# Optimization experiments

Hardware: AMD Instinct MI355X
Metric: run time of the kernel (lower is better)

## Reference

```python
import jax, jax.numpy as jnp
import numpy as np

B = 4096      # batch of users
D = 128       # embedding_dim
NA = 128      # num_anchors
AD = 128      # anchor_dim
NU = 100000   # num_users
NI = 50000    # num_items


def setup_inputs() -> dict:
    key = jax.random.key(0)
    ks = jax.random.split(key, 10)
    s = 0.05
    return {
        "user_indices": jax.random.randint(ks[0], (B,), 0, NU),
        "pos_item_indices": jax.random.randint(ks[1], (B,), 0, NI),
        "user_table": jax.random.normal(ks[2], (NU, D), dtype=jnp.float32) * s,
        "item_table": jax.random.normal(ks[3], (NI, D), dtype=jnp.float32) * s,
        "ln1_g": jnp.ones((D,), jnp.float32),
        "ln1_b": jnp.zeros((D,), jnp.float32),
        "send_W": jax.random.normal(ks[4], (D, AD), dtype=jnp.float32) * s,
        "send_a": jax.random.normal(ks[5], (2 * AD,), dtype=jnp.float32) * s,
        "anchors": jax.random.normal(ks[6], (NA, AD), dtype=jnp.float32) * s,
        "ln2_g": jnp.ones((NA,), jnp.float32),
        "ln2_b": jnp.zeros((NA,), jnp.float32),
        "recv_W": jax.random.normal(ks[7], (NA, D), dtype=jnp.float32) * s,
        "recv_a": jax.random.normal(ks[8], (2 * D,), dtype=jnp.float32) * s,
    }


def _layernorm(x, g, b, eps=1e-5):
    m = jnp.mean(x, axis=-1, keepdims=True)
    v = jnp.mean((x - m) ** 2, axis=-1, keepdims=True)
    return (x - m) * jax.lax.rsqrt(v + eps) * g + b


def _fca(x, W, a):
    # FullyConnectedAttention: score[i,j] = [t_i ; t_j] . a = t_i.a1 + t_j.a2
    # (decomposed form of the torch repeat/cat -> same math, no [B,B,2F] tensor)
    t = x @ W                       # [B, F]
    f = t.shape[-1]
    a1, a2 = a[:f], a[f:]
    e = (t @ a1)[:, None] + (t @ a2)[None, :]   # [B, B]
    w = jax.nn.softmax(e, axis=1)
    return w @ t                    # [B, F]


def reference(user_indices, pos_item_indices, user_table, item_table,
              ln1_g, ln1_b, send_W, send_a, anchors, ln2_g, ln2_b,
              recv_W, recv_a):
    u = user_table[user_indices]                 # [B, D]
    # AdaptiveAnchorConvolution
    nf = _layernorm(u, ln1_g, ln1_b)             # feature_norm
    sent = _fca(nf, send_W, send_a)              # send_attention -> [B, AD]
    ap = sent @ anchors.T                        # anchor projection [B, NA]
    na = _layernorm(ap, ln2_g, ln2_b)            # anchor_norm
    rec = _fca(na, recv_W, recv_a)               # receive_attention -> [B, D]
    ue = u + jnp.sin(rec)                        # residual + sin
    pos = item_table[pos_item_indices]           # [B, D]
    preds = ue @ item_table.T                    # [B, NI]
    return preds, ue, pos
```

## Files before the change

### kernel.cpp

```cpp
#include <hip/hip_runtime.h>
#include <hip/hip_bf16.h>

#define BB   4096
#define DD   128
#define NII  50000

typedef __attribute__((ext_vector_type(8))) short  bf8_t;
typedef __attribute__((ext_vector_type(4))) float  f4_t;
typedef __attribute__((ext_vector_type(4))) unsigned short us4_t;
typedef __attribute__((ext_vector_type(4))) float  fl4_t;

static __device__ __forceinline__ unsigned short f2bf(float f) {
    unsigned u = __float_as_uint(f);
    u += 0x7fffu + ((u >> 16) & 1u);
    return (unsigned short)(u >> 16);
}

static __device__ __forceinline__ void gload_lds16(const void* g, void* lds) {
    __builtin_amdgcn_global_load_lds(
        (const __attribute__((address_space(1))) void*)g,
        (__attribute__((address_space(3))) void*)lds, 16, 0, 0);
}

__global__ __launch_bounds__(128) void k1_embed_send(
    const int* __restrict__ uidx, const float* __restrict__ utab,
    const float* __restrict__ g1, const float* __restrict__ b1,
    const float* __restrict__ sendW, const float* __restrict__ senda,
    float* __restrict__ t_out, float* __restrict__ s2_out)
{
    __shared__ float sb[128];
    __shared__ float nf[128];
    const int row = blockIdx.x;
    const int tid = threadIdx.x;
    const long urow = uidx[row];
    const float x = utab[urow * 128 + tid];

    sb[tid] = x; __syncthreads();
    for (int s = 64; s > 0; s >>= 1) { if (tid < s) sb[tid] += sb[tid + s]; __syncthreads(); }
    const float mean = sb[0] * (1.0f / 128.0f); __syncthreads();
    const float dv = x - mean;
    sb[tid] = dv * dv; __syncthreads();
    for (int s = 64; s > 0; s >>= 1) { if (tid < s) sb[tid] += sb[tid + s]; __syncthreads(); }
    const float var = sb[0] * (1.0f / 128.0f);
    const float rs = rsqrtf(var + 1e-5f);
    nf[tid] = dv * rs * g1[tid] + b1[tid];
    __syncthreads();

    float acc = 0.f;
    #pragma unroll 8
    for (int d = 0; d < 128; ++d) acc += nf[d] * sendW[d * 128 + tid];
    t_out[row * 128 + tid] = acc;

    const float p = acc * senda[128 + tid];
    __syncthreads();
    sb[tid] = p; __syncthreads();
    for (int s = 64; s > 0; s >>= 1) { if (tid < s) sb[tid] += sb[tid + s]; __syncthreads(); }
    if (tid == 0) s2_out[row] = sb[0];
}

__global__ __launch_bounds__(256) void k2b_colsum(
    const float* __restrict__ t, const float* __restrict__ s2,
    float* __restrict__ partial)
{
    __shared__ float ew[128];
    __shared__ float sb[256];
    const int tid = threadIdx.x;

    float m = -1e30f;
    for (int i = tid; i < BB; i += 256) m = fmaxf(m, s2[i]);
    sb[tid] = m; __syncthreads();
    for (int s = 128; s > 0; s >>= 1) { if (tid < s) sb[tid] = fmaxf(sb[tid], sb[tid + s]); __syncthreads(); }
    m = sb[0]; __syncthreads();

    const int rbase = blockIdx.x * 128;
    if (tid < 128) ew[tid] = __expf(s2[rbase + tid] - m);
    __syncthreads();
    const int col = tid & 127, half = tid >> 7;
    float acc = 0.f;
    for (int j = half; j < 128; j += 2)
        acc += ew[j] * t[(rbase + j) * 128 + col];
    sb[tid] = acc; __syncthreads();
    if (tid < 128) partial[blockIdx.x * 128 + tid] = sb[tid] + sb[tid + 128];
}

__global__ __launch_bounds__(128) void k2c_finish(
    const float* __restrict__ partial, const float* __restrict__ s2,
    const float* __restrict__ anchors, const float* __restrict__ g2,
    const float* __restrict__ b2, const float* __restrict__ recvW,
    float* __restrict__ r_out)
{
    __shared__ float sent[128];
    __shared__ float na_s[128];
    __shared__ float sb[128];
    const int tid = threadIdx.x;

    float m = -1e30f;
    for (int i = tid; i < BB; i += 128) m = fmaxf(m, s2[i]);
    sb[tid] = m; __syncthreads();
    for (int s = 64; s > 0; s >>= 1) { if (tid < s) sb[tid] = fmaxf(sb[tid], sb[tid + s]); __syncthreads(); }
    m = sb[0]; __syncthreads();
    float sum = 0.f;
    for (int i = tid; i < BB; i += 128) sum += __expf(s2[i] - m);
    sb[tid] = sum; __syncthreads();
    for (int s = 64; s > 0; s >>= 1) { if (tid < s) sb[tid] += sb[tid + s]; __syncthreads(); }
    const float S = sb[0]; __syncthreads();

    float acc = 0.f;
    for (int b = 0; b < 32; ++b) acc += partial[b * 128 + tid];
    sent[tid] = acc / S;
    __syncthreads();
    float ap = 0.f;
    for (int c = 0; c < 128; ++c) ap += sent[c] * anchors[tid * 128 + c];
    sb[tid] = ap; __syncthreads();
    for (int s = 64; s > 0; s >>= 1) { if (tid < s) sb[tid] += sb[tid + s]; __syncthreads(); }
    const float mean = sb[0] * (1.0f / 128.0f); __syncthreads();
    const float dv = ap - mean;
    sb[tid] = dv * dv; __syncthreads();
    for (int s = 64; s > 0; s >>= 1) { if (tid < s) sb[tid] += sb[tid + s]; __syncthreads(); }
    const float var = sb[0] * (1.0f / 128.0f);
    const float rs = rsqrtf(var + 1e-5f);
    na_s[tid] = dv * rs * g2[tid] + b2[tid];
    __syncthreads();
    float t2 = 0.f;
    for (int k = 0; k < 128; ++k) t2 += na_s[k] * recvW[k * 128 + tid];
    r_out[tid] = sinf(t2);
}

__global__ __launch_bounds__(256) void k3_ue_pos(
    const int* __restrict__ uidx, const float* __restrict__ utab,
    const int* __restrict__ pidx, const float* __restrict__ itab,
    const float* __restrict__ r, float* __restrict__ ue_out,
    float* __restrict__ pos_out, unsigned short* __restrict__ uebf)
{
    const int gid = blockIdx.x * 256 + threadIdx.x;
    const int i = gid >> 7, d = gid & 127;
    const float rv = r[d];
    const float u = utab[(long)uidx[i] * 128 + d];
    const float ue = u + rv;
    ue_out[gid] = ue;
    uebf[gid] = f2bf(ue);
    pos_out[gid] = itab[(long)pidx[i] * 128 + d];
}

__global__ __launch_bounds__(256) void k3b_cvt_item(
    const float* __restrict__ itab, unsigned short* __restrict__ ibf)
{
    const int gid = blockIdx.x * 256 + threadIdx.x;
    const fl4_t v = *(const fl4_t*)(itab + (long)gid * 4);
    us4_t o;
    o.x = f2bf(v.x); o.y = f2bf(v.y); o.z = f2bf(v.z); o.w = f2bf(v.w);
    *(us4_t*)(ibf + (long)gid * 4) = o;
}

__global__ __launch_bounds__(512, 2) void k4_gemm(
    const unsigned short* __restrict__ uebf,
    const unsigned short* __restrict__ ibf,
    float* __restrict__ preds)
{
    __shared__ unsigned short lA[256 * 128];
    __shared__ unsigned short lB[256 * 128];

    const int tid = threadIdx.x;
    const int wave = tid >> 6, lane = tid & 63;
    const int l15 = lane & 15, kg = lane >> 4;
    const int col0 = blockIdx.x * 256;
    const int row0 = blockIdx.y * 256;

    #pragma unroll
    for (int i = 0; i < 8; ++i) {
        const int o  = (i * 512 + tid) * 16;
        const int r  = o >> 8;
        const int ch = (o >> 4) & 15;
        const int sw = ch ^ (r & 15);
        gload_lds16(uebf + (size_t)(row0 + r) * 128 + sw * 8,
                    (char*)lA + i * 8192 + wave * 1024);
        const int bc = (col0 + r) < NII ? (col0 + r) : (NII - 1);
        gload_lds16(ibf + (size_t)bc * 128 + sw * 8,
                    (char*)lB + i * 8192 + wave * 1024);
    }

    const int wr = wave >> 2, wcn = wave & 3;

    f4_t acc[8][4];
    #pragma unroll
    for (int m = 0; m < 8; ++m)
        #pragma unroll
        for (int n = 0; n < 4; ++n) acc[m][n] = (f4_t){0.f, 0.f, 0.f, 0.f};

    __syncthreads();

    #pragma unroll
    for (int kk = 0; kk < 4; ++kk) {
        const int c = kk * 4 + kg;
        bf8_t a[8], b[4];
        #pragma unroll
        for (int m = 0; m < 8; ++m) {
            const int r = wr * 128 + m * 16 + l15;
            a[m] = *(const bf8_t*)((const char*)lA + r * 256 + (c ^ (r & 15)) * 16);
        }
        #pragma unroll
        for (int n = 0; n < 4; ++n) {
            const int r = wcn * 64 + n * 16 + l15;
            b[n] = *(const bf8_t*)((const char*)lB + r * 256 + (c ^ (r & 15)) * 16);
        }
        #pragma unroll
        for (int m = 0; m < 8; ++m)
            #pragma unroll
            for (int n = 0; n < 4; ++n)
                acc[m][n] = __builtin_amdgcn_mfma_f32_16x16x32_bf16(b[n], a[m], acc[m][n], 0, 0, 0);
    }

    #pragma unroll
    for (int m = 0; m < 8; ++m) {
        const long grow = row0 + wr * 128 + m * 16 + l15;
        #pragma unroll
        for (int n = 0; n < 4; ++n) {
            const int gcol = col0 + wcn * 64 + n * 16 + kg * 4;
            if (gcol < NII)
                *(fl4_t*)(preds + grow * NII + gcol) = acc[m][n];
        }
    }
}

extern "C" void kernel_launch(void* const* d_in, const int* in_sizes, int n_in,
                              void* d_out, int out_size, void* d_ws, size_t ws_size,
                              hipStream_t stream) {
    const int*   uidx   = (const int*)  d_in[0];
    const int*   pidx   = (const int*)  d_in[1];
    const float* utab   = (const float*)d_in[2];
    const float* itab   = (const float*)d_in[3];
    const float* g1     = (const float*)d_in[4];
    const float* b1     = (const float*)d_in[5];
    const float* sendW  = (const float*)d_in[6];
    const float* senda  = (const float*)d_in[7];
    const float* anchors= (const float*)d_in[8];
    const float* g2     = (const float*)d_in[9];
    const float* b2     = (const float*)d_in[10];
    const float* recvW  = (const float*)d_in[11];

    char* ws = (char*)d_ws;
    float* t_ws    = (float*)(ws + 0);
    float* s2_ws   = (float*)(ws + 2097152);
    float* part_ws = (float*)(ws + 2113600);
    float* r_ws    = (float*)(ws + 2129984);
    unsigned short* uebf = (unsigned short*)(ws + 2130496);
    unsigned short* ibf  = (unsigned short*)(ws + 3179072);

    float* preds   = (float*)d_out;
    float* ue_out  = preds + (long)BB * NII;
    float* pos_out = ue_out + BB * DD;

    k3b_cvt_item<<<6250, 256, 0, stream>>>(itab, ibf);
    k1_embed_send<<<4096, 128, 0, stream>>>(uidx, utab, g1, b1, sendW, senda, t_ws, s2_ws);
    k2b_colsum<<<32, 256, 0, stream>>>(t_ws, s2_ws, part_ws);
    k2c_finish<<<1, 128, 0, stream>>>(part_ws, s2_ws, anchors, g2, b2, recvW, r_ws);
    k3_ue_pos<<<2048, 256, 0, stream>>>(uidx, utab, pidx, itab, r_ws, ue_out, pos_out, uebf);
    k4_gemm<<<dim3(196, 16, 1), 512, 0, stream>>>(uebf, ibf, preds);
}
```

Baseline: 243.4 us.

## Make GEMM blocks loop over item column tiles with double-buffered B prefetch

The preds GEMM now gives each block 4–5 consecutive 128-column item tiles instead of one 256-column tile. The block's 256-row user tile stays resident in LDS for the whole loop. The next item tile is prefetched into a second LDS buffer while the current tile's MFMAs and output stores run, synchronised with a partial vmcnt wait. The goal is to cut redundant A-tile loads, overlap B loads with compute and stores, and shrink the grid from 3136 to 1536 blocks to reduce tail imbalance. In exchange, each block does more serial work and relies on the hand-tuned vmcnt count being correct.

```diff
diff --git a/kernel.cpp b/kernel.cpp
--- a/kernel.cpp
+++ b/kernel.cpp
@@ -4,6 +4,7 @@
 #define BB   4096
 #define DD   128
 #define NII  50000
+#define NT128 391
 
 typedef __attribute__((ext_vector_type(8))) short  bf8_t;
 typedef __attribute__((ext_vector_type(4))) float  f4_t;
@@ -158,67 +159,93 @@
     float* __restrict__ preds)
 {
     __shared__ unsigned short lA[256 * 128];
-    __shared__ unsigned short lB[256 * 128];
+    __shared__ unsigned short lB[2][128 * 128];
 
     const int tid = threadIdx.x;
     const int wave = tid >> 6, lane = tid & 63;
     const int l15 = lane & 15, kg = lane >> 4;
-    const int col0 = blockIdx.x * 256;
+    const int bx = blockIdx.x;
     const int row0 = blockIdx.y * 256;
+    const int nt0 = bx * 4 + (bx < 7 ? bx : 7);
+    const int ns  = 4 + (bx < 7 ? 1 : 0);
 
     #pragma unroll
     for (int i = 0; i < 8; ++i) {
-        const int o  = (i * 512 + tid) * 16;
-        const int r  = o >> 8;
-        const int ch = (o >> 4) & 15;
-        const int sw = ch ^ (r & 15);
+        const int o = (i * 512 + tid) * 16, r = o >> 8, ch = (o >> 4) & 15, sw = ch ^ (r & 15);
         gload_lds16(uebf + (size_t)(row0 + r) * 128 + sw * 8,
                     (char*)lA + i * 8192 + wave * 1024);
-        const int bc = (col0 + r) < NII ? (col0 + r) : (NII - 1);
-        gload_lds16(ibf + (size_t)bc * 128 + sw * 8,
-                    (char*)lB + i * 8192 + wave * 1024);
     }
+    {
+        const int c0 = nt0 * 128;
+        #pragma unroll
+        for (int i = 0; i < 4; ++i) {
+            const int o = (i * 512 + tid) * 16, r = o >> 8, ch = (o >> 4) & 15, sw = ch ^ (r & 15);
+            const int bc = (c0 + r) < NII ? (c0 + r) : (NII - 1);
+            gload_lds16(ibf + (size_t)bc * 128 + sw * 8,
+                        (char*)lB[0] + i * 8192 + wave * 1024);
+        }
+    }
+    asm volatile("s_waitcnt vmcnt(0)" ::: "memory");
+    __builtin_amdgcn_sched_barrier(0);
+    __builtin_amdgcn_s_barrier();
 
     const int wr = wave >> 2, wcn = wave & 3;
 
-    f4_t acc[8][4];
-    #pragma unroll
-    for (int m = 0; m < 8; ++m)
-        #pragma unroll
-        for (int n = 0; n < 4; ++n) acc[m][n] = (f4_t){0.f, 0.f, 0.f, 0.f};
-
-    __syncthreads();
-
-    #pragma unroll
-    for (int kk = 0; kk < 4; ++kk) {
-        const int c = kk * 4 + kg;
-        bf8_t a[8], b[4];
+    for (int j = 0; j < ns; ++j) {
+        if (j + 1 < ns) {
+            const int c0n = (nt0 + j + 1) * 128;
+            char* dst = (char*)lB[(j + 1) & 1];
+            #pragma unroll
+            for (int i = 0; i < 4; ++i) {
+                const int o = (i * 512 + tid) * 16, r = o >> 8, ch = (o >> 4) & 15, sw = ch ^ (r & 15);
+                const int bc = (c0n + r) < NII ? (c0n + r) : (NII - 1);
+                gload_lds16(ibf + (size_t)bc * 128 + sw * 8, dst + i * 8192 + wave * 1024);
+            }
+        }
+        const unsigned short* bb = lB[j & 1];
+
+        f4_t acc[8][2];
+        #pragma unroll
+        for (int m = 0; m < 8; ++m)
+            #pragma unroll
+            for (int n = 0; n < 2; ++n) acc[m][n] = (f4_t){0.f, 0.f, 0.f, 0.f};
+
+        #pragma unroll
+        for (int kk = 0; kk < 4; ++kk) {
+            const int c = kk * 4 + kg;
+            bf8_t a[8], b[2];
+            #pragma unroll
+            for (int m = 0; m < 8; ++m) {
+                const int r = wr * 128 + m * 16 + l15;
+                a[m] = *(const bf8_t*)((const char*)lA + r * 256 + (c ^ (r & 15)) * 16);
+            }
+            #pragma unroll
+            for (int n = 0; n < 2; ++n) {
+                const int r = wcn * 32 + n * 16 + l15;
+                b[n] = *(const bf8_t*)((const char*)bb + r * 256 + (c ^ (r & 15)) * 16);
+            }
+            #pragma unroll
+            for (int m = 0; m < 8; ++m)
+                #pragma unroll
+                for (int n = 0; n < 2; ++n)
+                    acc[m][n] = __builtin_amdgcn_mfma_f32_16x16x32_bf16(b[n], a[m], acc[m][n], 0, 0, 0);
+        }
+
+        const int col0 = (nt0 + j) * 128;
         #pragma unroll
         for (int m = 0; m < 8; ++m) {
-            const int r = wr * 128 + m * 16 + l15;
-            a[m] = *(const bf8_t*)((const char*)lA + r * 256 + (c ^ (r & 15)) * 16);
-        }
-        #pragma unroll
-        for (int n = 0; n < 4; ++n) {
-            const int r = wcn * 64 + n * 16 + l15;
-            b[n] = *(const bf8_t*)((const char*)lB + r * 256 + (c ^ (r & 15)) * 16);
-        }
-        #pragma unroll
-        for (int m = 0; m < 8; ++m)
-            #pragma unroll
-            for (int n = 0; n < 4; ++n)
-                acc[m][n] = __builtin_amdgcn_mfma_f32_16x16x32_bf16(b[n], a[m], acc[m][n], 0, 0, 0);
-    }
-
-    #pragma unroll
-    for (int m = 0; m < 8; ++m) {
-        const long grow = row0 + wr * 128 + m * 16 + l15;
-        #pragma unroll
-        for (int n = 0; n < 4; ++n) {
-            const int gcol = col0 + wcn * 64 + n * 16 + kg * 4;
-            if (gcol < NII)
-                *(fl4_t*)(preds + grow * NII + gcol) = acc[m][n];
-        }
+            const long grow = row0 + wr * 128 + m * 16 + l15;
+            #pragma unroll
+            for (int n = 0; n < 2; ++n) {
+                const int gcol = col0 + wcn * 32 + n * 16 + kg * 4;
+                if (gcol < NII)
+                    *(fl4_t*)(preds + grow * NII + gcol) = acc[m][n];
+            }
+        }
+
+        asm volatile("s_waitcnt vmcnt(16)" ::: "memory");
+        __builtin_amdgcn_sched_barrier(0);
+        __builtin_amdgcn_s_barrier();
     }
 }
 
@@ -255,5 +282,5 @@
     k2b_colsum<<<32, 256, 0, stream>>>(t_ws, s2_ws, part_ws);
     k2c_finish<<<1, 128, 0, stream>>>(part_ws, s2_ws, anchors, g2, b2, recvW, r_ws);
     k3_ue_pos<<<2048, 256, 0, stream>>>(uidx, utab, pidx, itab, r_ws, ue_out, pos_out, uebf);
-    k4_gemm<<<dim3(196, 16, 1), 512, 0, stream>>>(uebf, ibf, preds);
-}
+    k4_gemm<<<dim3(96, 16, 1), 512, 0, stream>>>(uebf, ibf, preds);
+}
```

New measurement: 273.7 us. 12.5% more time.

## Stage GEMM epilogue through LDS for coalesced row stores; fuse item conversion into embed kernel

Applied to the files above, without the earlier changes.

The GEMM epilogue now writes each wave's accumulator tiles into LDS and reads them back so each store instruction covers contiguous 256-byte row segments of the large preds output, instead of scattered 16-byte chunks per row. Separately, the item-table bf16 conversion is merged into the embed/send kernel as extra blocks, removing one kernel launch. The epilogue adds a barrier and LDS round trips, and the shared buffer is reused after the main loop.

```diff
diff --git a/kernel.cpp b/kernel.cpp
--- a/kernel.cpp
+++ b/kernel.cpp
@@ -22,16 +22,30 @@
         (__attribute__((address_space(3))) void*)lds, 16, 0, 0);
 }
 
-__global__ __launch_bounds__(128) void k1_embed_send(
+__global__ __launch_bounds__(128) void kA_embed_cvt(
     const int* __restrict__ uidx, const float* __restrict__ utab,
     const float* __restrict__ g1, const float* __restrict__ b1,
     const float* __restrict__ sendW, const float* __restrict__ senda,
-    float* __restrict__ t_out, float* __restrict__ s2_out)
-{
+    const float* __restrict__ itab,
+    float* __restrict__ t_out, float* __restrict__ s2_out,
+    unsigned short* __restrict__ ibf)
+{
+    const int tid = threadIdx.x;
+    if (blockIdx.x >= BB) {
+        const long gid = ((long)(blockIdx.x - BB) * 128 + tid) * 2;
+        #pragma unroll
+        for (int h = 0; h < 2; ++h) {
+            const fl4_t v = *(const fl4_t*)(itab + (gid + h) * 4);
+            us4_t o;
+            o.x = f2bf(v.x); o.y = f2bf(v.y); o.z = f2bf(v.z); o.w = f2bf(v.w);
+            *(us4_t*)(ibf + (gid + h) * 4) = o;
+        }
+        return;
+    }
+
     __shared__ float sb[128];
     __shared__ float nf[128];
     const int row = blockIdx.x;
-    const int tid = threadIdx.x;
     const long urow = uidx[row];
     const float x = utab[urow * 128 + tid];
 
@@ -142,23 +156,14 @@
     pos_out[gid] = itab[(long)pidx[i] * 128 + d];
 }
 
-__global__ __launch_bounds__(256) void k3b_cvt_item(
-    const float* __restrict__ itab, unsigned short* __restrict__ ibf)
-{
-    const int gid = blockIdx.x * 256 + threadIdx.x;
-    const fl4_t v = *(const fl4_t*)(itab + (long)gid * 4);
-    us4_t o;
-    o.x = f2bf(v.x); o.y = f2bf(v.y); o.z = f2bf(v.z); o.w = f2bf(v.w);
-    *(us4_t*)(ibf + (long)gid * 4) = o;
-}
-
 __global__ __launch_bounds__(512, 2) void k4_gemm(
     const unsigned short* __restrict__ uebf,
     const unsigned short* __restrict__ ibf,
     float* __restrict__ preds)
 {
-    __shared__ unsigned short lA[256 * 128];
-    __shared__ unsigned short lB[256 * 128];
+    __shared__ char smem[131072];
+    unsigned short* lA = (unsigned short*)smem;
+    unsigned short* lB = (unsigned short*)(smem + 65536);
 
     const int tid = threadIdx.x;
     const int wave = tid >> 6, lane = tid & 63;
@@ -210,14 +215,28 @@
                 acc[m][n] = __builtin_amdgcn_mfma_f32_16x16x32_bf16(b[n], a[m], acc[m][n], 0, 0, 0);
     }
 
-    #pragma unroll
-    for (int m = 0; m < 8; ++m) {
-        const long grow = row0 + wr * 128 + m * 16 + l15;
-        #pragma unroll
-        for (int n = 0; n < 4; ++n) {
-            const int gcol = col0 + wcn * 64 + n * 16 + kg * 4;
+    __syncthreads();
+    float* ep = (float*)smem + wave * (32 * 76);
+
+    #pragma unroll
+    for (int h = 0; h < 4; ++h) {
+        #pragma unroll
+        for (int mm = 0; mm < 2; ++mm) {
+            const int m = h * 2 + mm;
+            #pragma unroll
+            for (int n = 0; n < 4; ++n)
+                #pragma unroll
+                for (int j = 0; j < 4; ++j)
+                    ep[(mm * 16 + l15) * 76 + n * 16 + kg * 4 + j] = acc[m][n][j];
+        }
+        #pragma unroll
+        for (int rr = 0; rr < 8; ++rr) {
+            const int lrow = rr * 4 + (lane >> 4);
+            const f4_t v = *(const f4_t*)(ep + lrow * 76 + (lane & 15) * 4);
+            const long grow = row0 + wr * 128 + h * 32 + lrow;
+            const int  gcol = col0 + wcn * 64 + (lane & 15) * 4;
             if (gcol < NII)
-                *(fl4_t*)(preds + grow * NII + gcol) = acc[m][n];
+                *(fl4_t*)(preds + grow * NII + gcol) = v;
         }
     }
 }
@@ -250,8 +269,8 @@
     float* ue_out  = preds + (long)BB * NII;
     float* pos_out = ue_out + BB * DD;
 
-    k3b_cvt_item<<<6250, 256, 0, stream>>>(itab, ibf);
-    k1_embed_send<<<4096, 128, 0, stream>>>(uidx, utab, g1, b1, sendW, senda, t_ws, s2_ws);
+    kA_embed_cvt<<<BB + 6250, 128, 0, stream>>>(uidx, utab, g1, b1, sendW, senda,
+                                                itab, t_ws, s2_ws, ibf);
     k2b_colsum<<<32, 256, 0, stream>>>(t_ws, s2_ws, part_ws);
     k2c_finish<<<1, 128, 0, stream>>>(part_ws, s2_ws, anchors, g2, b2, recvW, r_ws);
     k3_ue_pos<<<2048, 256, 0, stream>>>(uidx, utab, pidx, itab, r_ws, ue_out, pos_out, uebf);
```

Result: faster. 238.2 us, median of 2 (-2.1%).
